# Performance work log

Hardware: AMD Instinct MI355X
Metric: run time of the kernel (lower is better)

## Reference

```python
import jax, jax.numpy as jnp
import numpy as np

T, B, F, H = 2048, 50, 750, 100  # time, batch(seen by LSTM), input feat, hidden
OUT = 2

def setup_inputs() -> dict:
    key = jax.random.key(0)
    ks = jax.random.split(key, 7)
    s = 1.0 / np.sqrt(H)
    u = lambda k, shape: jax.random.uniform(k, shape, jnp.float32, -s, s)
    return {
        "x": jax.random.normal(ks[0], (T, B, F), jnp.float32),
        "W_ih": u(ks[1], (4 * H, F)),
        "W_hh": u(ks[2], (4 * H, H)),
        "b_ih": u(ks[3], (4 * H,)),
        "b_hh": u(ks[4], (4 * H,)),
        "fc_W": u(ks[5], (OUT, B * H)),
        "fc_b": u(ks[6], (OUT,)),
    }

def reference(x, W_ih, W_hh, b_ih, b_hh, fc_W, fc_b):
    # PyTorch LSTM (batch_first=False): scan over dim0. Gate order: i, f, g, o.
    # Precompute input projections for all steps at once: (T, B, 4H)
    x_proj = jnp.einsum('tbf,gf->tbg', x, W_ih) + b_ih + b_hh

    def step(carry, xp):
        h, c = carry                      # (B, H) each
        gates = xp + h @ W_hh.T           # (B, 4H)
        i, f, g, o = jnp.split(gates, 4, axis=-1)
        i = jax.nn.sigmoid(i)
        f = jax.nn.sigmoid(f)
        g = jnp.tanh(g)
        o = jax.nn.sigmoid(o)
        c = f * c + i * g
        h = o * jnp.tanh(c)
        return (h, c), h

    h0 = jnp.zeros((B, H), x.dtype)
    c0 = jnp.zeros((B, H), x.dtype)
    _, hs = jax.lax.scan(step, (h0, c0), x_proj)  # hs: (T, B, H)
    flat = hs.reshape(hs.shape[0], -1)            # (T, B*H) == (T, 5000)
    return flat @ fc_W.T + fc_b                   # (T, 2)
```

## Files before the change

kernel.cpp:

```cpp
#include <hip/hip_runtime.h>

#define T_DIM 2048
#define B_DIM 50
#define F_DIM 750
#define H_DIM 100
#define G4    400
#define M_DIM (T_DIM * B_DIM)
#define KPAD  768

typedef __attribute__((ext_vector_type(8))) short short8v;
typedef __attribute__((ext_vector_type(4))) float f32x4;
typedef __attribute__((ext_vector_type(2))) float f32x2;

__device__ __forceinline__ float fast_rcp(float x) { return __builtin_amdgcn_rcpf(x); }
__device__ __forceinline__ float tanh_f(float x) {
    return 1.0f - 2.0f * fast_rcp(__expf(2.0f * x) + 1.0f);
}

__device__ __forceinline__ unsigned short f2bf_rne(float f) {
    unsigned int u = __float_as_uint(f);
    u = (u + 0x7FFFu + ((u >> 16) & 1u)) >> 16;
    return (unsigned short)u;
}
__device__ __forceinline__ float bf2f(unsigned short h) {
    return __uint_as_float(((unsigned int)h) << 16);
}

template <int CTRL>
__device__ __forceinline__ float qperm(float x) {
    return __int_as_float(__builtin_amdgcn_mov_dpp(__float_as_int(x), CTRL, 0xF, 0xF, false));
}

__device__ __forceinline__ void lgkm_barrier() {
    __builtin_amdgcn_sched_barrier(0);
    asm volatile("s_waitcnt lgkmcnt(0)\ns_barrier" ::: "memory");
    __builtin_amdgcn_sched_barrier(0);
}

__global__ __launch_bounds__(256) void wconv(
    const float* __restrict__ W,
    unsigned short* __restrict__ Whi,
    unsigned short* __restrict__ Wlo)
{
    int i = blockIdx.x * 256 + threadIdx.x;
    if (i >= G4 * KPAD) return;
    int g = i / KPAD, k = i - g * KPAD;
    float v = (k < F_DIM) ? W[g * F_DIM + k] : 0.f;
    unsigned short h = f2bf_rne(v);
    Whi[i] = h;
    Wlo[i] = f2bf_rne(v - bf2f(h));
}

__global__ __launch_bounds__(512, 1) void xproj_mfma(
    const float* __restrict__ x,
    const unsigned short* __restrict__ Whi,
    const unsigned short* __restrict__ Wlo,
    const float* __restrict__ bih,
    const float* __restrict__ bhh,
    float* __restrict__ xp)
{
    const int m0   = blockIdx.x * 128;
    const int tid  = threadIdx.x;
    const int lane = tid & 63;
    const int w    = tid >> 6;
    const int rb   = (w >> 2) * 64;
    const int wc   = w & 3;
    const int fr   = lane & 15;
    const int fk   = (lane >> 4) * 8;

    __shared__ unsigned short Ahi[2][128][40];
    __shared__ unsigned short Alo[2][128][40];

    f32x4 acc[4][7];
    #pragma unroll
    for (int s = 0; s < 4; ++s)
        #pragma unroll
        for (int t = 0; t < 7; ++t)
            acc[s][t] = (f32x4){0.f, 0.f, 0.f, 0.f};

    float bias_t[7];
    #pragma unroll
    for (int tt = 0; tt < 7; ++tt) {
        const int nt = wc + 4 * tt;
        if (nt < 25) {
            const int n = nt * 16 + fr;
            bias_t[tt] = bih[n] + bhh[n];
        } else bias_t[tt] = 0.f;
    }

    const int sr = tid >> 2;
    const int sc = (tid & 3) * 8;
    const float* xrow = x + (size_t)(m0 + sr) * F_DIM;

    float f[8];

    #define STAGE_LOAD(KS)                                                     \
    {                                                                          \
        const int kg = (KS) * 32 + sc;                                         \
        _Pragma("unroll")                                                      \
        for (int i = 0; i < 8; i += 2) {                                       \
            if (kg + i + 1 < F_DIM) {                                          \
                float2 v = *reinterpret_cast<const float2*>(&xrow[kg + i]);    \
                f[i] = v.x; f[i + 1] = v.y;                                    \
            } else {                                                           \
                f[i]     = (kg + i < F_DIM) ? xrow[kg + i] : 0.f;              \
                f[i + 1] = 0.f;                                                \
            }                                                                  \
        }                                                                      \
    }

    #define STAGE_WRITE(NB)                                                    \
    {                                                                          \
        short8v vh, vl;                                                        \
        _Pragma("unroll")                                                      \
        for (int i = 0; i < 8; ++i) {                                          \
            unsigned int u = __float_as_uint(f[i]);                            \
            vh[i] = (short)(u >> 16);                                          \
            float r = f[i] - __uint_as_float(u & 0xffff0000u);                 \
            vl[i] = (short)(__float_as_uint(r) >> 16);                         \
        }                                                                      \
        *reinterpret_cast<short8v*>(&Ahi[NB][sr][sc]) = vh;                    \
        *reinterpret_cast<short8v*>(&Alo[NB][sr][sc]) = vl;                    \
    }

    STAGE_LOAD(0);
    STAGE_WRITE(0);
    lgkm_barrier();

    for (int s = 0; s < 24; ++s) {
        const int cur = s & 1;
        short8v ah[4], al[4];
        #pragma unroll
        for (int st = 0; st < 4; ++st) {
            ah[st] = *reinterpret_cast<const short8v*>(&Ahi[cur][rb + st * 16 + fr][fk]);
            al[st] = *reinterpret_cast<const short8v*>(&Alo[cur][rb + st * 16 + fr][fk]);
        }

        if (s < 23) STAGE_LOAD(s + 1);

        const int kb = s * 32 + fk;
        #pragma unroll
        for (int tt = 0; tt < 7; ++tt) {
            const int nt = wc + 4 * tt;
            if (nt < 25) {
                const int n = nt * 16 + fr;
                const short8v bh = *reinterpret_cast<const short8v*>(&Whi[n * KPAD + kb]);
                const short8v bl = *reinterpret_cast<const short8v*>(&Wlo[n * KPAD + kb]);
                #pragma unroll
                for (int st = 0; st < 4; ++st) {
                    acc[st][tt] = __builtin_amdgcn_mfma_f32_16x16x32_bf16(ah[st], bh, acc[st][tt], 0, 0, 0);
                    acc[st][tt] = __builtin_amdgcn_mfma_f32_16x16x32_bf16(ah[st], bl, acc[st][tt], 0, 0, 0);
                    acc[st][tt] = __builtin_amdgcn_mfma_f32_16x16x32_bf16(al[st], bh, acc[st][tt], 0, 0, 0);
                }
            }
        }

        if (s < 23) STAGE_WRITE(cur ^ 1);
        lgkm_barrier();
    }

    #pragma unroll
    for (int tt = 0; tt < 7; ++tt) {
        const int nt = wc + 4 * tt;
        if (nt < 25) {
            const int n = nt * 16 + fr;
            #pragma unroll
            for (int st = 0; st < 4; ++st) {
                #pragma unroll
                for (int r = 0; r < 4; ++r) {
                    const int m = m0 + rb + st * 16 + (lane >> 4) * 4 + r;
                    xp[(size_t)m * G4 + n] = acc[st][tt][r] + bias_t[tt];
                }
            }
        }
    }
    #undef STAGE_LOAD
    #undef STAGE_WRITE
}

__global__ __launch_bounds__(448, 1) void lstm_scan(
    const float* __restrict__ xp,
    const float* __restrict__ Whh,
    float* __restrict__ hs)
{
    const int b   = blockIdx.x;
    const int tid = threadIdx.x;
    const int g   = tid & 3;
    const int j   = tid >> 2;
    const int jc  = (j < H_DIM) ? j : (H_DIM - 1);
    const int row = g * H_DIM + jc;

    __shared__ __align__(16) float hbuf[2][H_DIM];

    f32x2 w2[50];
    {
        const float* wrow = Whh + (size_t)row * H_DIM;
        #pragma unroll
        for (int i = 0; i < 25; ++i) {
            float4 v = *reinterpret_cast<const float4*>(&wrow[4 * i]);
            w2[2 * i]     = (f32x2){v.x, v.y};
            w2[2 * i + 1] = (f32x2){v.z, v.w};
        }
    }

    if (tid < H_DIM) { hbuf[0][tid] = 0.f; hbuf[1][tid] = 0.f; }

    const bool writer = (g == 0) && (j < H_DIM);

    const float s_act = (g == 2) ? 2.0f : 1.0f;
    const float nsl2  = -s_act * 1.44269504088896f;
    const float nsm1  = 1.0f - s_act;

    float c = 0.f;
    const float* xp_ptr = xp + (size_t)b * G4 + row;
    float*       hs_ptr = hs + (size_t)b * H_DIM + jc;
    const size_t xstride = (size_t)B_DIM * G4;

    float xpv   = xp_ptr[0];
    float xp_n1 = xp_ptr[xstride];
    __syncthreads();

    int p = 0;
    for (int t = 0; t < T_DIM; ++t) {
        float xp_n2 = 0.f;
        if (t + 2 < T_DIM) xp_n2 = xp_ptr[2 * xstride];
        xp_ptr += xstride;

        f32x2 a0 = {xpv, 0.f};
        f32x2 a1 = {0.f, 0.f};
        const float* hb = hbuf[p];
        #pragma unroll
        for (int k = 0; k < 25; ++k) {
            float4 hv = *reinterpret_cast<const float4*>(&hb[4 * k]);
            a0 = __builtin_elementwise_fma(w2[2 * k],     (f32x2){hv.x, hv.y}, a0);
            a1 = __builtin_elementwise_fma(w2[2 * k + 1], (f32x2){hv.z, hv.w}, a1);
        }
        const float pre = (a0.x + a0.y) + (a1.x + a1.y);

        const float act = fmaf(s_act,
            fast_rcp(1.0f + __builtin_amdgcn_exp2f(nsl2 * pre)), nsm1);

        const float i_ = qperm<0x00>(act);
        const float f_ = qperm<0x55>(act);
        const float g_ = qperm<0xAA>(act);
        const float o_ = qperm<0xFF>(act);

        c = fmaf(f_, c, i_ * g_);
        const float h = o_ * tanh_f(c);

        if (writer) {
            hbuf[p ^ 1][jc] = h;
            *hs_ptr = h;
        }
        hs_ptr += B_DIM * H_DIM;
        lgkm_barrier();
        p ^= 1;
        xpv   = xp_n1;
        xp_n1 = xp_n2;
    }
}

__global__ __launch_bounds__(256) void fc_kernel(
    const float* __restrict__ hs,
    const float* __restrict__ fcW,
    const float* __restrict__ fcb,
    float* __restrict__ out)
{
    const int t   = blockIdx.x;
    const int tid = threadIdx.x;

    float p0 = 0.f, p1 = 0.f;
    for (int k = tid * 4; k < 5000; k += 1024) {
        const float4 hv = *reinterpret_cast<const float4*>(&hs[(size_t)t * 5000 + k]);
        const float4 w0 = *reinterpret_cast<const float4*>(&fcW[k]);
        const float4 w1 = *reinterpret_cast<const float4*>(&fcW[5000 + k]);
        p0 += hv.x * w0.x + hv.y * w0.y + hv.z * w0.z + hv.w * w0.w;
        p1 += hv.x * w1.x + hv.y * w1.y + hv.z * w1.z + hv.w * w1.w;
    }
    #pragma unroll
    for (int off = 32; off > 0; off >>= 1) {
        p0 += __shfl_xor(p0, off);
        p1 += __shfl_xor(p1, off);
    }
    __shared__ float red[8];
    const int wv = tid >> 6;
    if ((tid & 63) == 0) { red[wv * 2] = p0; red[wv * 2 + 1] = p1; }
    __syncthreads();
    if (tid == 0) {
        out[2 * t]     = fcb[0] + red[0] + red[2] + red[4] + red[6];
        out[2 * t + 1] = fcb[1] + red[1] + red[3] + red[5] + red[7];
    }
}

extern "C" void kernel_launch(void* const* d_in, const int* in_sizes, int n_in,
                              void* d_out, int out_size, void* d_ws, size_t ws_size,
                              hipStream_t stream) {
    const float* x   = (const float*)d_in[0];
    const float* Wih = (const float*)d_in[1];
    const float* Whh = (const float*)d_in[2];
    const float* bih = (const float*)d_in[3];
    const float* bhh = (const float*)d_in[4];
    const float* fcW = (const float*)d_in[5];
    const float* fcb = (const float*)d_in[6];
    float* out = (float*)d_out;

    char* ws = (char*)d_ws;
    float*          xp  = (float*)ws;
    unsigned short* Whi = (unsigned short*)(ws + (size_t)M_DIM * G4 * 4);
    unsigned short* Wlo = Whi + (size_t)G4 * KPAD;
    float*          hs  = (float*)((char*)(Wlo + (size_t)G4 * KPAD));

    wconv<<<(G4 * KPAD + 255) / 256, 256, 0, stream>>>(Wih, Whi, Wlo);

    xproj_mfma<<<M_DIM / 128, 512, 0, stream>>>(x, Whi, Wlo, bih, bhh, xp);

    lstm_scan<<<B_DIM, 448, 0, stream>>>(xp, Whh, hs);

    fc_kernel<<<T_DIM, 256, 0, stream>>>(hs, fcW, fcb, out);
}
```

Measured before the change: 1.646 ms.

## Split recurrent dot products across quad lanes with packed Whh layout

Repacks W_hh so each of the four lanes in a quad holds a quarter of the hidden-state inputs for all four gates of one hidden unit. Each lane then reads only 28 padded h values from LDS per step instead of 100, computes four partial gate sums, and combines them with quad permute reductions. The goal is to cut LDS read traffic and shorten the per-step critical path of the serial scan, at the cost of extra cross-lane shuffles, selects, a small extra packing kernel and a padded h buffer layout. It also relaxes the occupancy hint to waves_per_eu(1,2).

```diff
diff --git a/kernel.cpp b/kernel.cpp
--- a/kernel.cpp
+++ b/kernel.cpp
@@ -49,6 +49,18 @@
     unsigned short h = f2bf_rne(v);
     Whi[i] = h;
     Wlo[i] = f2bf_rne(v - bf2f(h));
+}
+
+__global__ __launch_bounds__(256) void whh_pack(
+    const float* __restrict__ Whh,
+    float* __restrict__ wpack)
+{
+    int i = blockIdx.x * 256 + threadIdx.x;
+    if (i >= 400 * 112) return;
+    int lane = i / 112, rem = i - lane * 112;
+    int g = rem / 28, r = rem - g * 28;
+    int j = lane >> 2, q = lane & 3;
+    wpack[i] = (r < 25) ? Whh[(size_t)(g * H_DIM + j) * H_DIM + 25 * q + r] : 0.f;
 }
 
 __global__ __launch_bounds__(512, 1) void xproj_mfma(
@@ -178,36 +190,38 @@
     #undef STAGE_WRITE
 }
 
-__global__ __launch_bounds__(448, 1) void lstm_scan(
+__global__ __attribute__((amdgpu_waves_per_eu(1, 2))) __launch_bounds__(448)
+void lstm_scan(
     const float* __restrict__ xp,
-    const float* __restrict__ Whh,
+    const float* __restrict__ wpack,
     float* __restrict__ hs)
 {
     const int b   = blockIdx.x;
     const int tid = threadIdx.x;
-    const int g   = tid & 3;
+    const int q   = tid & 3;
     const int j   = tid >> 2;
     const int jc  = (j < H_DIM) ? j : (H_DIM - 1);
-    const int row = g * H_DIM + jc;
-
-    __shared__ __align__(16) float hbuf[2][H_DIM];
-
-    f32x2 w2[50];
+    const int row = q * H_DIM + jc;
+
+    __shared__ __align__(16) float hbuf[2][112];
+
+    f32x2 w2[56];
     {
-        const float* wrow = Whh + (size_t)row * H_DIM;
-        #pragma unroll
-        for (int i = 0; i < 25; ++i) {
-            float4 v = *reinterpret_cast<const float4*>(&wrow[4 * i]);
+        const float* wb = wpack + (size_t)((jc << 2) + q) * 112;
+        #pragma unroll
+        for (int i = 0; i < 28; ++i) {
+            float4 v = *reinterpret_cast<const float4*>(&wb[4 * i]);
             w2[2 * i]     = (f32x2){v.x, v.y};
             w2[2 * i + 1] = (f32x2){v.z, v.w};
         }
     }
 
-    if (tid < H_DIM) { hbuf[0][tid] = 0.f; hbuf[1][tid] = 0.f; }
-
-    const bool writer = (g == 0) && (j < H_DIM);
-
-    const float s_act = (g == 2) ? 2.0f : 1.0f;
+    if (tid < 112) { hbuf[0][tid] = 0.f; hbuf[1][tid] = 0.f; }
+
+    const int hpos = (jc / 25) * 28 + (jc % 25);
+    const bool writer = (q == 0) && (j < H_DIM);
+
+    const float s_act = (q == 2) ? 2.0f : 1.0f;
     const float nsl2  = -s_act * 1.44269504088896f;
     const float nsm1  = 1.0f - s_act;
 
@@ -226,17 +240,43 @@
         if (t + 2 < T_DIM) xp_n2 = xp_ptr[2 * xstride];
         xp_ptr += xstride;
 
-        f32x2 a0 = {xpv, 0.f};
-        f32x2 a1 = {0.f, 0.f};
-        const float* hb = hbuf[p];
-        #pragma unroll
-        for (int k = 0; k < 25; ++k) {
-            float4 hv = *reinterpret_cast<const float4*>(&hb[4 * k]);
-            a0 = __builtin_elementwise_fma(w2[2 * k],     (f32x2){hv.x, hv.y}, a0);
-            a1 = __builtin_elementwise_fma(w2[2 * k + 1], (f32x2){hv.z, hv.w}, a1);
-        }
-        const float pre = (a0.x + a0.y) + (a1.x + a1.y);
-
+        f32x2 a0 = {(q == 0) ? xpv : 0.f, 0.f};
+        f32x2 a1 = {(q == 1) ? xpv : 0.f, 0.f};
+        f32x2 a2 = {(q == 2) ? xpv : 0.f, 0.f};
+        f32x2 a3 = {(q == 3) ? xpv : 0.f, 0.f};
+        const float* hq = &hbuf[p][28 * q];
+        #pragma unroll
+        for (int k = 0; k < 7; ++k) {
+            float4 hv = *reinterpret_cast<const float4*>(hq + 4 * k);
+            f32x2 hlo = {hv.x, hv.y};
+            f32x2 hhi = {hv.z, hv.w};
+            a0 = __builtin_elementwise_fma(w2[2 * k],          hlo, a0);
+            a0 = __builtin_elementwise_fma(w2[2 * k + 1],      hhi, a0);
+            a1 = __builtin_elementwise_fma(w2[14 + 2 * k],     hlo, a1);
+            a1 = __builtin_elementwise_fma(w2[14 + 2 * k + 1], hhi, a1);
+            a2 = __builtin_elementwise_fma(w2[28 + 2 * k],     hlo, a2);
+            a2 = __builtin_elementwise_fma(w2[28 + 2 * k + 1], hhi, a2);
+            a3 = __builtin_elementwise_fma(w2[42 + 2 * k],     hlo, a3);
+            a3 = __builtin_elementwise_fma(w2[42 + 2 * k + 1], hhi, a3);
+        }
+        float ac0 = a0.x + a0.y;
+        float ac1 = a1.x + a1.y;
+        float ac2 = a2.x + a2.y;
+        float ac3 = a3.x + a3.y;
+
+        ac0 += qperm<0xB1>(ac0);
+        ac1 += qperm<0xB1>(ac1);
+        ac2 += qperm<0xB1>(ac2);
+        ac3 += qperm<0xB1>(ac3);
+        ac0 += qperm<0x4E>(ac0);
+        ac1 += qperm<0x4E>(ac1);
+        ac2 += qperm<0x4E>(ac2);
+        ac3 += qperm<0x4E>(ac3);
+
+        float pre = ac0;
+        pre = (q == 1) ? ac1 : pre;
+        pre = (q == 2) ? ac2 : pre;
+        pre = (q == 3) ? ac3 : pre;
         const float act = fmaf(s_act,
             fast_rcp(1.0f + __builtin_amdgcn_exp2f(nsl2 * pre)), nsm1);
 
@@ -249,7 +289,7 @@
         const float h = o_ * tanh_f(c);
 
         if (writer) {
-            hbuf[p ^ 1][jc] = h;
+            hbuf[p ^ 1][hpos] = h;
             *hs_ptr = h;
         }
         hs_ptr += B_DIM * H_DIM;
@@ -305,16 +345,18 @@
     float* out = (float*)d_out;
 
     char* ws = (char*)d_ws;
-    float*          xp  = (float*)ws;
-    unsigned short* Whi = (unsigned short*)(ws + (size_t)M_DIM * G4 * 4);
-    unsigned short* Wlo = Whi + (size_t)G4 * KPAD;
-    float*          hs  = (float*)((char*)(Wlo + (size_t)G4 * KPAD));
+    float*          xp    = (float*)ws;
+    unsigned short* Whi   = (unsigned short*)(ws + (size_t)M_DIM * G4 * 4);
+    unsigned short* Wlo   = Whi + (size_t)G4 * KPAD;
+    float*          hs    = (float*)((char*)(Wlo + (size_t)G4 * KPAD));
+    float*          wpack = hs + (size_t)M_DIM * H_DIM;
 
     wconv<<<(G4 * KPAD + 255) / 256, 256, 0, stream>>>(Wih, Whi, Wlo);
+    whh_pack<<<(400 * 112 + 255) / 256, 256, 0, stream>>>(Whh, wpack);
 
     xproj_mfma<<<M_DIM / 128, 512, 0, stream>>>(x, Whi, Wlo, bih, bhh, xp);
 
-    lstm_scan<<<B_DIM, 448, 0, stream>>>(xp, Whh, hs);
+    lstm_scan<<<B_DIM, 448, 0, stream>>>(xp, wpack, hs);
 
     fc_kernel<<<T_DIM, 256, 0, stream>>>(hs, fcW, fcb, out);
 }
```

After: 1.615 ms. About the same (-1.9%).

## Split LSTM recurrent dot product across two lanes per gate row

Applied to the files above, without the earlier changes.

The recurrent matvec in the scan kernel is split so each gate row's 100-element dot product is computed by two lanes of 50 elements each, then combined with a ds_swizzle xor-4 reduction. W_hh is pre-packed by a new small kernel into a padded per-lane layout, and the block size grows from 448 to 832 threads. A large unused shared array is declared to force one block per CU. This halves the serial FMA chain per step at the cost of an extra cross-lane exchange and more waves per barrier.

```diff
diff --git a/kernel.cpp b/kernel.cpp
--- a/kernel.cpp
+++ b/kernel.cpp
@@ -30,6 +30,9 @@
 __device__ __forceinline__ float qperm(float x) {
     return __int_as_float(__builtin_amdgcn_mov_dpp(__float_as_int(x), CTRL, 0xF, 0xF, false));
 }
+__device__ __forceinline__ float swz_xor4(float x) {
+    return __int_as_float(__builtin_amdgcn_ds_swizzle(__float_as_int(x), 0x101F));
+}
 
 __device__ __forceinline__ void lgkm_barrier() {
     __builtin_amdgcn_sched_barrier(0);
@@ -49,6 +52,18 @@
     unsigned short h = f2bf_rne(v);
     Whi[i] = h;
     Wlo[i] = f2bf_rne(v - bf2f(h));
+}
+
+__global__ __launch_bounds__(256) void whh_pack(
+    const float* __restrict__ Whh,
+    float* __restrict__ wpack)
+{
+    int i = blockIdx.x * 256 + threadIdx.x;
+    if (i >= 800 * 56) return;
+    int lane = i / 56, r = i - lane * 56;
+    int half = lane & 1, qj = lane >> 1;
+    int q = qj & 3, j = qj >> 2;
+    wpack[i] = (r < 50) ? Whh[(size_t)(q * H_DIM + j) * H_DIM + 50 * half + r] : 0.f;
 }
 
 __global__ __launch_bounds__(512, 1) void xproj_mfma(
@@ -178,36 +193,45 @@
     #undef STAGE_WRITE
 }
 
-__global__ __launch_bounds__(448, 1) void lstm_scan(
+__global__ __launch_bounds__(832, 1) void lstm_scan(
     const float* __restrict__ xp,
-    const float* __restrict__ Whh,
+    const float* __restrict__ wpack,
     float* __restrict__ hs)
 {
-    const int b   = blockIdx.x;
-    const int tid = threadIdx.x;
-    const int g   = tid & 3;
-    const int j   = tid >> 2;
-    const int jc  = (j < H_DIM) ? j : (H_DIM - 1);
-    const int row = g * H_DIM + jc;
-
-    __shared__ __align__(16) float hbuf[2][H_DIM];
-
-    f32x2 w2[50];
+    const int b    = blockIdx.x;
+    const int tid  = threadIdx.x;
+    const int oct  = tid & 7;
+    const int q    = oct & 3;
+    const int half = oct >> 2;
+    const int j    = tid >> 3;
+    const int jc   = (j < H_DIM) ? j : (H_DIM - 1);
+    const int row  = q * H_DIM + jc;
+
+    __shared__ __align__(16) float hbuf[2][112];
+    __shared__ float lds_occupancy_brake[37000];
+
+    if (b >= B_DIM) {
+        lds_occupancy_brake[tid] = (float)tid;
+        hbuf[0][tid & 1] = lds_occupancy_brake[(tid * 7) & 1023];
+    }
+
+    f32x2 w2[28];
     {
-        const float* wrow = Whh + (size_t)row * H_DIM;
-        #pragma unroll
-        for (int i = 0; i < 25; ++i) {
-            float4 v = *reinterpret_cast<const float4*>(&wrow[4 * i]);
+        const float* wb = wpack + (size_t)(((jc << 2) + q) * 2 + half) * 56;
+        #pragma unroll
+        for (int i = 0; i < 14; ++i) {
+            float4 v = *reinterpret_cast<const float4*>(&wb[4 * i]);
             w2[2 * i]     = (f32x2){v.x, v.y};
             w2[2 * i + 1] = (f32x2){v.z, v.w};
         }
     }
 
-    if (tid < H_DIM) { hbuf[0][tid] = 0.f; hbuf[1][tid] = 0.f; }
-
-    const bool writer = (g == 0) && (j < H_DIM);
-
-    const float s_act = (g == 2) ? 2.0f : 1.0f;
+    if (tid < 112) { hbuf[0][tid] = 0.f; hbuf[1][tid] = 0.f; }
+
+    const int hslot = (jc < 50) ? jc : (56 + jc - 50);
+    const bool writer = (oct == 0) && (j < H_DIM);
+
+    const float s_act = (q == 2) ? 2.0f : 1.0f;
     const float nsl2  = -s_act * 1.44269504088896f;
     const float nsm1  = 1.0f - s_act;
 
@@ -226,19 +250,24 @@
         if (t + 2 < T_DIM) xp_n2 = xp_ptr[2 * xstride];
         xp_ptr += xstride;
 
-        f32x2 a0 = {xpv, 0.f};
+        f32x2 a0 = {(half == 0) ? xpv : 0.f, 0.f};
         f32x2 a1 = {0.f, 0.f};
-        const float* hb = hbuf[p];
-        #pragma unroll
-        for (int k = 0; k < 25; ++k) {
-            float4 hv = *reinterpret_cast<const float4*>(&hb[4 * k]);
-            a0 = __builtin_elementwise_fma(w2[2 * k],     (f32x2){hv.x, hv.y}, a0);
-            a1 = __builtin_elementwise_fma(w2[2 * k + 1], (f32x2){hv.z, hv.w}, a1);
-        }
-        const float pre = (a0.x + a0.y) + (a1.x + a1.y);
+        const float* hq = &hbuf[p][half * 56];
+        #pragma unroll
+        for (int k = 0; k < 7; ++k) {
+            float4 hv0 = *reinterpret_cast<const float4*>(hq + 8 * k);
+            float4 hv1 = *reinterpret_cast<const float4*>(hq + 8 * k + 4);
+            a0 = __builtin_elementwise_fma(w2[4 * k],     (f32x2){hv0.x, hv0.y}, a0);
+            a0 = __builtin_elementwise_fma(w2[4 * k + 1], (f32x2){hv0.z, hv0.w}, a0);
+            a1 = __builtin_elementwise_fma(w2[4 * k + 2], (f32x2){hv1.x, hv1.y}, a1);
+            a1 = __builtin_elementwise_fma(w2[4 * k + 3], (f32x2){hv1.z, hv1.w}, a1);
+        }
+        float ac = (a0.x + a0.y) + (a1.x + a1.y);
+
+        ac += swz_xor4(ac);
 
         const float act = fmaf(s_act,
-            fast_rcp(1.0f + __builtin_amdgcn_exp2f(nsl2 * pre)), nsm1);
+            fast_rcp(1.0f + __builtin_amdgcn_exp2f(nsl2 * ac)), nsm1);
 
         const float i_ = qperm<0x00>(act);
         const float f_ = qperm<0x55>(act);
@@ -249,7 +278,7 @@
         const float h = o_ * tanh_f(c);
 
         if (writer) {
-            hbuf[p ^ 1][jc] = h;
+            hbuf[p ^ 1][hslot] = h;
             *hs_ptr = h;
         }
         hs_ptr += B_DIM * H_DIM;
@@ -305,16 +334,18 @@
     float* out = (float*)d_out;
 
     char* ws = (char*)d_ws;
-    float*          xp  = (float*)ws;
-    unsigned short* Whi = (unsigned short*)(ws + (size_t)M_DIM * G4 * 4);
-    unsigned short* Wlo = Whi + (size_t)G4 * KPAD;
-    float*          hs  = (float*)((char*)(Wlo + (size_t)G4 * KPAD));
+    float*          xp    = (float*)ws;
+    unsigned short* Whi   = (unsigned short*)(ws + (size_t)M_DIM * G4 * 4);
+    unsigned short* Wlo   = Whi + (size_t)G4 * KPAD;
+    float*          hs    = (float*)((char*)(Wlo + (size_t)G4 * KPAD));
+    float*          wpack = hs + (size_t)M_DIM * H_DIM;
 
     wconv<<<(G4 * KPAD + 255) / 256, 256, 0, stream>>>(Wih, Whi, Wlo);
+    whh_pack<<<(800 * 56 + 255) / 256, 256, 0, stream>>>(Whh, wpack);
 
     xproj_mfma<<<M_DIM / 128, 512, 0, stream>>>(x, Whi, Wlo, bih, bhh, xp);
 
-    lstm_scan<<<B_DIM, 448, 0, stream>>>(xp, Whh, hs);
+    lstm_scan<<<B_DIM, 832, 0, stream>>>(xp, wpack, hs);
 
     fc_kernel<<<T_DIM, 256, 0, stream>>>(hs, fcW, fcb, out);
 }
```

Measured after the change: 1.858 ms. 1.13x slower.
